# Kernel optimization log

Measured on AMD Instinct MI355X. Metric: run time of the kernel, lower is better.

## Reference

```python
import jax, jax.numpy as jnp
import numpy as np

N_NODES = 100000
N_EDGES = 1600000
IN_CH = 128
EMB = 64


def _init_linear(key, fan_in, fan_out):
    kw, kb = jax.random.split(key)
    scale = 1.0 / np.sqrt(fan_in)
    W = jax.random.uniform(kw, (fan_in, fan_out), jnp.float32, -scale, scale)
    b = jax.random.uniform(kb, (fan_out,), jnp.float32, -scale, scale)
    return W, b


def setup_inputs() -> dict:
    key = jax.random.key(0)
    ks = jax.random.split(key, 6)
    x = jax.random.normal(ks[0], (N_NODES, IN_CH), jnp.float32)
    edge_index = jax.random.randint(ks[1], (2, N_EDGES), 0, N_NODES)
    batch = jnp.zeros((N_NODES,), jnp.int32)
    # conv1 MLP: in_channels -> 32 -> 64 ; conv2 MLP: 64 -> 64 -> embedding_dim
    W1, b1 = _init_linear(ks[2], IN_CH, 32)
    W2, b2 = _init_linear(ks[3], 32, 64)
    W3, b3 = _init_linear(ks[4], 64, 64)
    W4, b4 = _init_linear(ks[5], 64, EMB)
    return {"x": x, "edge_index": edge_index, "batch": batch,
            "W1": W1, "b1": b1, "W2": W2, "b2": b2,
            "W3": W3, "b3": b3, "W4": W4, "b4": b4}


def _mlp(h, Wa, ba, Wb, bb):
    # PyG MLP: Linear -> act -> Linear (plain last layer)
    return jax.nn.relu(h @ Wa + ba) @ Wb + bb


def _gin_conv(x, src, dst, Wa, ba, Wb, bb):
    # out_i = MLP((1+eps)*x_i + sum_{j->i} x_j), eps = 0 (GINConv default)
    agg = jax.ops.segment_sum(x[src], dst, num_segments=N_NODES)  # [N, d]
    return _mlp(x + agg, Wa, ba, Wb, bb)


def reference(x, edge_index, batch, W1, b1, W2, b2, W3, b3, W4, b4):
    src, dst = edge_index[0], edge_index[1]
    h = jax.nn.relu(_gin_conv(x, src, dst, W1, b1, W2, b2))  # [N, 64]
    h = jax.nn.relu(_gin_conv(h, src, dst, W3, b3, W4, b4))  # [N, EMB]
    # batch is overwritten with zeros in the original forward -> single graph
    pooled = jnp.mean(h, axis=0, keepdims=True)  # [1, EMB]
    return h, pooled
```

## Files before the change

### kernel.cpp

```cpp
#include <hip/hip_runtime.h>

#define NN 100000
#define NE 1600000
#define NLB 256
#define CHUNK (NE / NLB)
#define NB 196
#define BN 512
#define NTILE (NN / 32)

__device__ __forceinline__ float bf2f(unsigned short u) {
    return __uint_as_float(((unsigned int)u) << 16);
}
__device__ __forceinline__ unsigned short f2bf(float f) {
    unsigned int u = __float_as_uint(f);
    return (unsigned short)((u + 0x7FFFu + ((u >> 16) & 1u)) >> 16);
}

__global__ __launch_bounds__(256) void k_front(const int* __restrict__ src,
                                               const int* __restrict__ dst,
                                               int* __restrict__ pairs,
                                               int* __restrict__ tstart,
                                               int* __restrict__ tcnt,
                                               int* __restrict__ btot,
                                               const float* __restrict__ x,
                                               const float* __restrict__ W1,
                                               unsigned short* __restrict__ z1) {
    __shared__ float Ws[128 * 32];
    __shared__ float xs[32][129];
    __shared__ int cnt[NB];
    __shared__ int sc[256];
    __shared__ int cur[NB];
    int tid = threadIdx.x;
    if (blockIdx.x < NLB) {
        int blk = blockIdx.x;
        int e0 = blk * CHUNK;
        for (int i = tid; i < NB; i += 256) cnt[i] = 0;
        __syncthreads();
        for (int i = tid; i < CHUNK; i += 256) atomicAdd(&cnt[dst[e0 + i] >> 9], 1);
        __syncthreads();
        sc[tid] = (tid < NB) ? cnt[tid] : 0;
        __syncthreads();
        for (int off = 1; off < 256; off <<= 1) {
            int v = (tid >= off) ? sc[tid - off] : 0;
            __syncthreads();
            sc[tid] += v;
            __syncthreads();
        }
        if (tid < NB) {
            int excl = sc[tid] - cnt[tid];
            cur[tid] = excl;
            tstart[blk * NB + tid] = excl;
            tcnt[blk * NB + tid]   = cnt[tid];
            atomicAdd(&btot[tid], cnt[tid]);
        }
        __syncthreads();
        for (int i = tid; i < CHUNK; i += 256) {
            int d = dst[e0 + i], s = src[e0 + i];
            int p = atomicAdd(&cur[d >> 9], 1);
            pairs[e0 + p] = ((d & (BN - 1)) << 17) | s;
        }
    } else {
        int base = (blockIdx.x - NLB) * 32;
        for (int i = tid; i < 1024; i += 256) {
            float4 w = ((const float4*)W1)[i];
            float* d = &Ws[i * 4];
            d[0] = w.x; d[1] = w.y; d[2] = w.z; d[3] = w.w;
        }
        for (int t = tid; t < 1024; t += 256) {
            int n = t >> 5, c = t & 31;
            float4 v = ((const float4*)(x + (size_t)(base + n) * 128))[c];
            float* d = &xs[n][c * 4];
            d[0] = v.x; d[1] = v.y; d[2] = v.z; d[3] = v.w;
        }
        __syncthreads();
        int n_loc = tid >> 3;
        int j0    = (tid & 7) * 4;
        float a0 = 0.f, a1 = 0.f, a2 = 0.f, a3 = 0.f;
        #pragma unroll 8
        for (int k = 0; k < 128; k++) {
            float xv = xs[n_loc][k];
            float4 w = *(const float4*)&Ws[k * 32 + j0];
            a0 = fmaf(xv, w.x, a0); a1 = fmaf(xv, w.y, a1);
            a2 = fmaf(xv, w.z, a2); a3 = fmaf(xv, w.w, a3);
        }
        ushort4 o = { f2bf(a0), f2bf(a1), f2bf(a2), f2bf(a3) };
        *(ushort4*)&z1[(size_t)(base + n_loc) * 32 + j0] = o;
    }
}

__global__ __launch_bounds__(1024) void k_build(const int* __restrict__ pairs,
                                                const int* __restrict__ tstart,
                                                const int* __restrict__ tcnt,
                                                const int* __restrict__ btot,
                                                int* __restrict__ csr,
                                                int* __restrict__ row) {
    __shared__ int segS[NLB], segL[NLB];
    __shared__ int ncnt[BN];
    __shared__ int nbase[BN + 1];
    __shared__ int sc[256];
    __shared__ int sc2[256];
    __shared__ int base_s;
    int tid = threadIdx.x, b = blockIdx.x;

    if (tid < 256) sc2[tid] = (tid < NB) ? btot[tid] : 0;
    __syncthreads();
    for (int off = 1; off < 256; off <<= 1) {
        int v = 0;
        if (tid < 256 && tid >= off) v = sc2[tid - off];
        __syncthreads();
        if (tid < 256) sc2[tid] += v;
        __syncthreads();
    }
    if (tid == 0) base_s = (b == 0) ? 0 : sc2[b - 1];
    if (tid < NLB) {
        segS[tid] = tid * CHUNK + tstart[tid * NB + b];
        segL[tid] = tcnt[tid * NB + b];
    }
    for (int i = tid; i < BN; i += 1024) ncnt[i] = 0;
    __syncthreads();

    int wave = tid >> 6, lane = tid & 63;
    for (int s = wave; s < NLB; s += 16) {
        int st = segS[s], len = segL[s];
        for (int i = lane; i < len; i += 64)
            atomicAdd(&ncnt[pairs[st + i] >> 17], 1);
    }
    __syncthreads();

    int c0 = 0, c1 = 0, tsum = 0;
    if (tid < 256) { c0 = ncnt[2 * tid]; c1 = ncnt[2 * tid + 1]; tsum = c0 + c1; sc[tid] = tsum; }
    __syncthreads();
    for (int off = 1; off < 256; off <<= 1) {
        int v = 0;
        if (tid < 256 && tid >= off) v = sc[tid - off];
        __syncthreads();
        if (tid < 256) sc[tid] += v;
        __syncthreads();
    }
    if (tid < 256) {
        int excl = sc[tid] - tsum;
        nbase[2 * tid]     = excl;
        nbase[2 * tid + 1] = excl + c0;
    }
    __syncthreads();

    int base = base_s;
    if (tid < BN) {
        int n = b * BN + tid;
        if (n < NN) row[n] = base + nbase[tid];
        ncnt[tid] = 0;
    }
    if (b == NB - 1 && tid == 0) row[NN] = NE;
    __syncthreads();

    for (int s = wave; s < NLB; s += 16) {
        int st = segS[s], len = segL[s];
        for (int i = lane; i < len; i += 64) {
            int p = pairs[st + i];
            int ln = p >> 17;
            int pos = atomicAdd(&ncnt[ln], 1);
            csr[base + nbase[ln] + pos] = p & 0x1FFFF;
        }
    }
}

__global__ __launch_bounds__(256) void k_gather32(const int* __restrict__ row,
                                                  const int* __restrict__ csr,
                                                  const unsigned short* __restrict__ z,
                                                  float* __restrict__ agg) {
    int n = blockIdx.x * 4 + (threadIdx.x >> 6);
    int lane = threadIdx.x & 63;
    int g = lane >> 3;
    int q = lane & 7;
    int j = row[n], e = row[n + 1];
    float a0 = 0.f, a1 = 0.f, a2 = 0.f, a3 = 0.f;
#define G32_BODY(J) { \
        int idx_ = csr[(J) + g]; \
        uint2 v_ = *(const uint2*)(z + (size_t)idx_ * 32 + q * 4); \
        a0 += __uint_as_float(v_.x << 16); \
        a1 += __uint_as_float(v_.x & 0xFFFF0000u); \
        a2 += __uint_as_float(v_.y << 16); \
        a3 += __uint_as_float(v_.y & 0xFFFF0000u); }
    for (; j + 16 <= e; j += 16) { G32_BODY(j) G32_BODY(j + 8) }
    if (j + 8 <= e) { G32_BODY(j) j += 8; }
    int rem = e - j;
    if (rem > 0) {
        int gg = (g < rem) ? g : (rem - 1);
        int idx_ = csr[j + gg];
        uint2 v_ = *(const uint2*)(z + (size_t)idx_ * 32 + q * 4);
        if (g < rem) {
            a0 += __uint_as_float(v_.x << 16);
            a1 += __uint_as_float(v_.x & 0xFFFF0000u);
            a2 += __uint_as_float(v_.y << 16);
            a3 += __uint_as_float(v_.y & 0xFFFF0000u);
        }
    }
#undef G32_BODY
    #pragma unroll
    for (int m = 8; m < 64; m <<= 1) {
        a0 += __shfl_xor(a0, m);
        a1 += __shfl_xor(a1, m);
        a2 += __shfl_xor(a2, m);
        a3 += __shfl_xor(a3, m);
    }
    if (g == 0) *(float4*)&agg[(size_t)n * 32 + q * 4] = make_float4(a0, a1, a2, a3);
}

__global__ __launch_bounds__(256) void k_gather64(const int* __restrict__ row,
                                                  const int* __restrict__ csr,
                                                  const unsigned short* __restrict__ z,
                                                  float* __restrict__ agg) {
    int n = blockIdx.x * 4 + (threadIdx.x >> 6);
    int lane = threadIdx.x & 63;
    int g = lane >> 3;
    int q = lane & 7;
    int j = row[n], e = row[n + 1];
    float a0 = 0.f, a1 = 0.f, a2 = 0.f, a3 = 0.f;
    float a4 = 0.f, a5 = 0.f, a6 = 0.f, a7 = 0.f;
#define G64B(J) { \
        int idx_ = csr[(J) + g]; \
        uint4 v_ = *(const uint4*)(z + (size_t)idx_ * 64 + q * 8); \
        a0 += __uint_as_float(v_.x << 16); a1 += __uint_as_float(v_.x & 0xFFFF0000u); \
        a2 += __uint_as_float(v_.y << 16); a3 += __uint_as_float(v_.y & 0xFFFF0000u); \
        a4 += __uint_as_float(v_.z << 16); a5 += __uint_as_float(v_.z & 0xFFFF0000u); \
        a6 += __uint_as_float(v_.w << 16); a7 += __uint_as_float(v_.w & 0xFFFF0000u); }
    for (; j + 16 <= e; j += 16) { G64B(j) G64B(j + 8) }
    if (j + 8 <= e) { G64B(j) j += 8; }
    int rem = e - j;
    if (rem > 0) {
        int gg = (g < rem) ? g : (rem - 1);
        int idx_ = csr[j + gg];
        uint4 v_ = *(const uint4*)(z + (size_t)idx_ * 64 + q * 8);
        if (g < rem) {
            a0 += __uint_as_float(v_.x << 16); a1 += __uint_as_float(v_.x & 0xFFFF0000u);
            a2 += __uint_as_float(v_.y << 16); a3 += __uint_as_float(v_.y & 0xFFFF0000u);
            a4 += __uint_as_float(v_.z << 16); a5 += __uint_as_float(v_.z & 0xFFFF0000u);
            a6 += __uint_as_float(v_.w << 16); a7 += __uint_as_float(v_.w & 0xFFFF0000u);
        }
    }
#undef G64B
    #pragma unroll
    for (int m = 8; m < 64; m <<= 1) {
        a0 += __shfl_xor(a0, m); a1 += __shfl_xor(a1, m);
        a2 += __shfl_xor(a2, m); a3 += __shfl_xor(a3, m);
        a4 += __shfl_xor(a4, m); a5 += __shfl_xor(a5, m);
        a6 += __shfl_xor(a6, m); a7 += __shfl_xor(a7, m);
    }
    if (g == 0) {
        *(float4*)&agg[(size_t)n * 64 + q * 8]     = make_float4(a0, a1, a2, a3);
        *(float4*)&agg[(size_t)n * 64 + q * 8 + 4] = make_float4(a4, a5, a6, a7);
    }
}

__global__ __launch_bounds__(256) void k_mid(const unsigned short* __restrict__ z1,
                                             const float* __restrict__ agg1,
                                             const float* __restrict__ b1,
                                             const float* __restrict__ W2,
                                             const float* __restrict__ b2,
                                             const float* __restrict__ W3,
                                             unsigned short* __restrict__ z2) {
    __shared__ float W2s[32 * 64];
    __shared__ float W3s[64 * 64];
    __shared__ float ts[32][33];
    __shared__ float hs[32 * 68];
    __shared__ float b1s[32], b2s[64];
    int tid = threadIdx.x;
    int base = blockIdx.x * 32;
    for (int i = tid; i < 512; i += 256) {
        float4 w = ((const float4*)W2)[i];
        float* d = &W2s[i * 4];
        d[0] = w.x; d[1] = w.y; d[2] = w.z; d[3] = w.w;
    }
    for (int i = tid; i < 1024; i += 256) {
        float4 w = ((const float4*)W3)[i];
        float* d = &W3s[i * 4];
        d[0] = w.x; d[1] = w.y; d[2] = w.z; d[3] = w.w;
    }
    if (tid < 32) b1s[tid] = b1[tid];
    if (tid >= 64 && tid < 128) b2s[tid - 64] = b2[tid - 64];
    __syncthreads();
    #pragma unroll
    for (int r = 0; r < 4; r++) {
        int idx = tid + 256 * r;
        int n = idx >> 5, f = idx & 31;
        ts[n][f] = fmaxf(bf2f(z1[(size_t)base * 32 + idx]) + agg1[(size_t)base * 32 + idx] + b1s[f], 0.f);
    }
    __syncthreads();
    int n2 = tid >> 4;
    int j0 = (tid & 15) * 4;
    int na = 2 * n2, nb = 2 * n2 + 1;
    {
        float a00=0,a01=0,a02=0,a03=0,a10=0,a11=0,a12=0,a13=0;
        #pragma unroll 8
        for (int k = 0; k < 32; k++) {
            float t0 = ts[na][k], t1 = ts[nb][k];
            float4 w = *(const float4*)&W2s[k * 64 + j0];
            a00=fmaf(t0,w.x,a00); a01=fmaf(t0,w.y,a01); a02=fmaf(t0,w.z,a02); a03=fmaf(t0,w.w,a03);
            a10=fmaf(t1,w.x,a10); a11=fmaf(t1,w.y,a11); a12=fmaf(t1,w.z,a12); a13=fmaf(t1,w.w,a13);
        }
        *(float4*)&hs[na * 68 + j0] = make_float4(fmaxf(a00+b2s[j0],0.f), fmaxf(a01+b2s[j0+1],0.f),
                                                  fmaxf(a02+b2s[j0+2],0.f), fmaxf(a03+b2s[j0+3],0.f));
        *(float4*)&hs[nb * 68 + j0] = make_float4(fmaxf(a10+b2s[j0],0.f), fmaxf(a11+b2s[j0+1],0.f),
                                                  fmaxf(a12+b2s[j0+2],0.f), fmaxf(a13+b2s[j0+3],0.f));
    }
    __syncthreads();
    {
        float a00=0,a01=0,a02=0,a03=0,a10=0,a11=0,a12=0,a13=0;
        #pragma unroll 8
        for (int k = 0; k < 64; k++) {
            float h0 = hs[na * 68 + k], h1 = hs[nb * 68 + k];
            float4 w = *(const float4*)&W3s[k * 64 + j0];
            a00=fmaf(h0,w.x,a00); a01=fmaf(h0,w.y,a01); a02=fmaf(h0,w.z,a02); a03=fmaf(h0,w.w,a03);
            a10=fmaf(h1,w.x,a10); a11=fmaf(h1,w.y,a11); a12=fmaf(h1,w.z,a12); a13=fmaf(h1,w.w,a13);
        }
        ushort4 oa = { f2bf(a00), f2bf(a01), f2bf(a02), f2bf(a03) };
        ushort4 ob = { f2bf(a10), f2bf(a11), f2bf(a12), f2bf(a13) };
        *(ushort4*)&z2[(size_t)(base + na) * 64 + j0] = oa;
        *(ushort4*)&z2[(size_t)(base + nb) * 64 + j0] = ob;
    }
}

__global__ __launch_bounds__(256) void k_final(const unsigned short* __restrict__ z2,
                                               const float* __restrict__ agg2,
                                               const float* __restrict__ b3,
                                               const float* __restrict__ W4,
                                               const float* __restrict__ b4,
                                               float* __restrict__ out,
                                               float* __restrict__ gpool) {
    __shared__ float W4s[64 * 64];
    __shared__ float us[32 * 68];
    __shared__ float b3s[64], b4s[64], pool[64];
    int tid = threadIdx.x;
    int base = blockIdx.x * 32;
    for (int i = tid; i < 1024; i += 256) {
        float4 w = ((const float4*)W4)[i];
        float* d = &W4s[i * 4];
        d[0] = w.x; d[1] = w.y; d[2] = w.z; d[3] = w.w;
    }
    if (tid < 64) { b3s[tid] = b3[tid]; pool[tid] = 0.f; }
    if (tid >= 64 && tid < 128) b4s[tid - 64] = b4[tid - 64];
    __syncthreads();
    #pragma unroll
    for (int r = 0; r < 8; r++) {
        int idx = tid + 256 * r;
        int n = idx >> 6, f = idx & 63;
        us[n * 68 + f] = fmaxf(bf2f(z2[(size_t)base * 64 + idx]) + agg2[(size_t)base * 64 + idx] + b3s[f], 0.f);
    }
    __syncthreads();
    int n2 = tid >> 4;
    int j0 = (tid & 15) * 4;
    int na = 2 * n2, nb = 2 * n2 + 1;
    float a00=0,a01=0,a02=0,a03=0,a10=0,a11=0,a12=0,a13=0;
    #pragma unroll 8
    for (int k = 0; k < 64; k++) {
        float u0 = us[na * 68 + k], u1 = us[nb * 68 + k];
        float4 w = *(const float4*)&W4s[k * 64 + j0];
        a00=fmaf(u0,w.x,a00); a01=fmaf(u0,w.y,a01); a02=fmaf(u0,w.z,a02); a03=fmaf(u0,w.w,a03);
        a10=fmaf(u1,w.x,a10); a11=fmaf(u1,w.y,a11); a12=fmaf(u1,w.z,a12); a13=fmaf(u1,w.w,a13);
    }
    float v00=fmaxf(a00+b4s[j0],0.f), v01=fmaxf(a01+b4s[j0+1],0.f);
    float v02=fmaxf(a02+b4s[j0+2],0.f), v03=fmaxf(a03+b4s[j0+3],0.f);
    float v10=fmaxf(a10+b4s[j0],0.f), v11=fmaxf(a11+b4s[j0+1],0.f);
    float v12=fmaxf(a12+b4s[j0+2],0.f), v13=fmaxf(a13+b4s[j0+3],0.f);
    *(float4*)&out[(size_t)(base + na) * 64 + j0] = make_float4(v00, v01, v02, v03);
    *(float4*)&out[(size_t)(base + nb) * 64 + j0] = make_float4(v10, v11, v12, v13);
    __syncthreads();
    atomicAdd(&pool[j0 + 0], v00 + v10);
    atomicAdd(&pool[j0 + 1], v01 + v11);
    atomicAdd(&pool[j0 + 2], v02 + v12);
    atomicAdd(&pool[j0 + 3], v03 + v13);
    __syncthreads();
    if (tid < 64) unsafeAtomicAdd(&gpool[(blockIdx.x & 7) * 64 + tid], pool[tid]);
}

__global__ void k_pool(const float* __restrict__ gpool, float* __restrict__ out) {
    int t = threadIdx.x;
    if (t < 64) {
        float s = 0.f;
        #pragma unroll
        for (int k = 0; k < 8; k++) s += gpool[k * 64 + t];
        out[(size_t)NN * 64 + t] = s * (1.0f / NN);
    }
}

extern "C" void kernel_launch(void* const* d_in, const int* in_sizes, int n_in,
                              void* d_out, int out_size, void* d_ws, size_t ws_size,
                              hipStream_t stream) {
    const float* x  = (const float*)d_in[0];
    const int*   ei = (const int*)d_in[1];
    const float* W1 = (const float*)d_in[3];
    const float* b1 = (const float*)d_in[4];
    const float* W2 = (const float*)d_in[5];
    const float* b2 = (const float*)d_in[6];
    const float* W3 = (const float*)d_in[7];
    const float* b3 = (const float*)d_in[8];
    const float* W4 = (const float*)d_in[9];
    const float* b4 = (const float*)d_in[10];
    float* out = (float*)d_out;

    int*   ip     = (int*)d_ws;
    int*   tstart = ip;
    int*   tcnt   = ip + NLB * NB;
    int*   btot   = ip + 2 * NLB * NB;
    float* gpool  = (float*)(ip + 2 * NLB * NB + 196);
    int*   row    = ip + 2 * NLB * NB + 196 + 512;
    int*   csr    = row + NN + 4;
    int*   pairs  = csr + NE;
    unsigned short* z1b = (unsigned short*)(pairs + NE);
    float* agg1   = (float*)(pairs + NE + NN * 16);
    float* agg2   = (float*)pairs;
    unsigned short* z2b = (unsigned short*)(agg1 + (size_t)NN * 32);
    const int* src = ei;
    const int* dst = ei + NE;

    hipMemsetAsync(btot, 0, (196 + 512) * sizeof(int), stream);
    k_front<<<NLB + NTILE, 256, 0, stream>>>(src, dst, pairs, tstart, tcnt, btot, x, W1, z1b);
    k_build<<<NB, 1024, 0, stream>>>(pairs, tstart, tcnt, btot, csr, row);
    k_gather32<<<NN / 4, 256, 0, stream>>>(row, csr, z1b, agg1);
    k_mid<<<NTILE, 256, 0, stream>>>(z1b, agg1, b1, W2, b2, W3, z2b);
    k_gather64<<<NN / 4, 256, 0, stream>>>(row, csr, z2b, agg2);
    k_final<<<NTILE, 256, 0, stream>>>(z2b, agg2, b3, W4, b4, out, gpool);
    k_pool<<<1, 64, 0, stream>>>(gpool, out);
}
```

Measured before the change: 304.0 us.

## Compute two nodes per thread in front GEMM, loading x directly into registers

```diff
diff --git a/kernel.cpp b/kernel.cpp
--- a/kernel.cpp
+++ b/kernel.cpp
@@ -7,6 +7,7 @@
 #define NB 196
 #define BN 512
 #define NTILE (NN / 32)
+#define NFT 1563
 
 __device__ __forceinline__ float bf2f(unsigned short u) {
     return __uint_as_float(((unsigned int)u) << 16);
@@ -26,7 +27,6 @@
                                                const float* __restrict__ W1,
                                                unsigned short* __restrict__ z1) {
     __shared__ float Ws[128 * 32];
-    __shared__ float xs[32][129];
     __shared__ int cnt[NB];
     __shared__ int sc[256];
     __shared__ int cur[NB];
@@ -60,31 +60,46 @@
             pairs[e0 + p] = ((d & (BN - 1)) << 17) | s;
         }
     } else {
-        int base = (blockIdx.x - NLB) * 32;
+        int base = (blockIdx.x - NLB) * 64;
         for (int i = tid; i < 1024; i += 256) {
             float4 w = ((const float4*)W1)[i];
             float* d = &Ws[i * 4];
             d[0] = w.x; d[1] = w.y; d[2] = w.z; d[3] = w.w;
         }
-        for (int t = tid; t < 1024; t += 256) {
-            int n = t >> 5, c = t & 31;
-            float4 v = ((const float4*)(x + (size_t)(base + n) * 128))[c];
-            float* d = &xs[n][c * 4];
-            d[0] = v.x; d[1] = v.y; d[2] = v.z; d[3] = v.w;
-        }
-        __syncthreads();
-        int n_loc = tid >> 3;
-        int j0    = (tid & 7) * 4;
-        float a0 = 0.f, a1 = 0.f, a2 = 0.f, a3 = 0.f;
-        #pragma unroll 8
-        for (int k = 0; k < 128; k++) {
-            float xv = xs[n_loc][k];
-            float4 w = *(const float4*)&Ws[k * 32 + j0];
-            a0 = fmaf(xv, w.x, a0); a1 = fmaf(xv, w.y, a1);
-            a2 = fmaf(xv, w.z, a2); a3 = fmaf(xv, w.w, a3);
-        }
-        ushort4 o = { f2bf(a0), f2bf(a1), f2bf(a2), f2bf(a3) };
-        *(ushort4*)&z1[(size_t)(base + n_loc) * 32 + j0] = o;
+        __syncthreads();
+        int pair = tid >> 3;
+        int j0   = (tid & 7) * 4;
+        int na = base + pair * 2;
+        int nb = na + 1;
+        int ca = (na < NN) ? na : (NN - 1);
+        int cb = (nb < NN) ? nb : (NN - 1);
+        const float4* xa4 = (const float4*)(x + (size_t)ca * 128);
+        const float4* xb4 = (const float4*)(x + (size_t)cb * 128);
+        float a00=0,a01=0,a02=0,a03=0,a10=0,a11=0,a12=0,a13=0;
+        #pragma unroll
+        for (int c = 0; c < 4; c++) {
+            float4 ra[8], rb[8];
+            #pragma unroll
+            for (int i = 0; i < 8; i++) { ra[i] = xa4[c * 8 + i]; rb[i] = xb4[c * 8 + i]; }
+            #pragma unroll
+            for (int i = 0; i < 8; i++) {
+                #pragma unroll
+                for (int kk = 0; kk < 4; kk++) {
+                    int k = c * 32 + i * 4 + kk;
+                    float4 w = *(const float4*)&Ws[k * 32 + j0];
+                    float xv_a = (&ra[i].x)[kk];
+                    float xv_b = (&rb[i].x)[kk];
+                    a00 = fmaf(xv_a, w.x, a00); a01 = fmaf(xv_a, w.y, a01);
+                    a02 = fmaf(xv_a, w.z, a02); a03 = fmaf(xv_a, w.w, a03);
+                    a10 = fmaf(xv_b, w.x, a10); a11 = fmaf(xv_b, w.y, a11);
+                    a12 = fmaf(xv_b, w.z, a12); a13 = fmaf(xv_b, w.w, a13);
+                }
+            }
+        }
+        ushort4 oa = { f2bf(a00), f2bf(a01), f2bf(a02), f2bf(a03) };
+        ushort4 ob = { f2bf(a10), f2bf(a11), f2bf(a12), f2bf(a13) };
+        if (na < NN) *(ushort4*)&z1[(size_t)na * 32 + j0] = oa;
+        if (nb < NN) *(ushort4*)&z1[(size_t)nb * 32 + j0] = ob;
     }
 }
 
@@ -414,7 +429,7 @@
     const int* dst = ei + NE;
 
     hipMemsetAsync(btot, 0, (196 + 512) * sizeof(int), stream);
-    k_front<<<NLB + NTILE, 256, 0, stream>>>(src, dst, pairs, tstart, tcnt, btot, x, W1, z1b);
+    k_front<<<NLB + NFT, 256, 0, stream>>>(src, dst, pairs, tstart, tcnt, btot, x, W1, z1b);
     k_build<<<NB, 1024, 0, stream>>>(pairs, tstart, tcnt, btot, csr, row);
     k_gather32<<<NN / 4, 256, 0, stream>>>(row, csr, z1b, agg1);
     k_mid<<<NTILE, 256, 0, stream>>>(z1b, agg1, b1, W2, b2, W3, z2b);
```

Result: slower. 581.2 us (+91.2%).
